# Performance work log

Measured on AMD Instinct MI355X. Metric: run time of the kernel, lower is better.

## Reference

```python
import jax, jax.numpy as jnp
import numpy as np

B, N, D, NFP, L = 4096, 64, 128, 2048, 3  # graphs, nodes/graph, emb_dim, vocab, layers


def setup_inputs() -> dict:
    key = jax.random.key(0)
    k0, k1, k2, k3, k4 = jax.random.split(key, 5)
    fps = jax.random.randint(k0, (B * N,), 0, NFP)            # node fingerprint ids, all graphs concatenated
    adj = jax.random.uniform(k1, (B, N, N), dtype=jnp.float32)  # per-graph adjacency blocks
    emb = jax.random.normal(k2, (NFP, D), dtype=jnp.float32) * 0.02
    W = jax.random.normal(k3, (L, D, D), dtype=jnp.float32) / np.sqrt(D).astype(np.float32)
    b = jax.random.normal(k4, (L, D), dtype=jnp.float32) * 0.01
    return {"fps": fps, "adj": adj, "emb": emb, "W": W, "b": b}


def reference(fps, adj, emb, W, b):
    # h = self.emb(fps): gather, then view as [B, N, D] so the block-diagonal
    # adjs.mm becomes an exact batched matmul over the true graph blocks.
    h = emb[fps].reshape(B, N, D)
    for l in range(L):
        # z = relu(W_l h + b_l); torch Linear is x @ W^T + b
        z = jax.nn.relu(jnp.einsum('bnd,kd->bnk', h, W[l]) + b[l])
        # h = z + adjs.mm(z), restricted to the diagonal blocks (same math)
        h = z + jnp.einsum('bmn,bnd->bmd', adj, z)
    # split by sz_list and sum each chunk -> per-graph sum pooling
    return h.sum(axis=1)  # [B, D]
```

## Files before the change

### kernel.cpp

```cpp
#include <hip/hip_runtime.h>

#define NGRAPH 4096
#define NNODE  64
#define NDIM   128
#define NLAYER 3
#define PH 136

typedef __attribute__((ext_vector_type(8))) short short8;
typedef __attribute__((ext_vector_type(4))) float f32x4;
typedef __bf16 bf16x2 __attribute__((ext_vector_type(2)));

union S8 { short8 s8; unsigned d[4]; };

static __device__ inline ushort f2bf(float f) {
  unsigned u = __float_as_uint(f);
  u += 0x7FFF + ((u >> 16) & 1);
  return (ushort)(u >> 16);
}

static __device__ inline unsigned pkbf(float x, float y) {
#if __has_builtin(__builtin_amdgcn_cvt_pk_bf16_f32)
  bf16x2 v = __builtin_amdgcn_cvt_pk_bf16_f32(x, y);
  return __builtin_bit_cast(unsigned, v);
#else
  return (unsigned)f2bf(x) | ((unsigned)f2bf(y) << 16);
#endif
}

__device__ __align__(16) ushort g_wbf[NLAYER * NDIM * NDIM];

__global__ __launch_bounds__(256) void convert_w(const float* __restrict__ W) {
  int i = blockIdx.x * 256 + threadIdx.x;
  g_wbf[i] = f2bf(W[i]);
}

__global__ __launch_bounds__(256, 4) void mpnn_mfma(
    const int* __restrict__ fps, const float* __restrict__ adj,
    const float* __restrict__ emb, const float* __restrict__ bias,
    float* __restrict__ out) {
  __shared__ __align__(16) ushort sh0[NNODE * PH];
  __shared__ __align__(16) ushort sh1[NNODE * PH];

  const int g    = blockIdx.x;
  const int t    = threadIdx.x;
  const int w    = t >> 6;
  const int lane = t & 63;
  const int r    = lane & 15;
  const int q    = lane >> 4;
  const int n0   = w << 5;

  const int addr0 = (r + 32 * (q & 1)) << 2;
  const int addr1 = addr0 + 64;
  const bool hiQ  = (q >= 2);

  const int* fg = fps + g * NNODE;
#pragma unroll
  for (int it = 0; it < 8; ++it) {
    int idx = it * 256 + t;
    int n = idx >> 5;
    int c = (idx & 31) << 2;
    float4 v = *(const float4*)(emb + fg[n] * NDIM + c);
    uint2 u = {pkbf(v.x, v.y), pkbf(v.z, v.w)};
    *(uint2*)(sh0 + n * PH + c) = u;
  }

  const float* adjg = adj + (size_t)g * NNODE * NNODE;
  short8 fadj[4][2];
#pragma unroll
  for (int nt = 0; nt < 4; ++nt) {
    int row = nt * 16 + r;
    const float* rp = adjg + row * NNODE;
#pragma unroll
    for (int kh = 0; kh < 2; ++kh) {
      int cb = kh * 32 + 8 * q;
      float4 v0 = *(const float4*)(rp + cb);
      float4 v1 = *(const float4*)(rp + cb + 4);
      float vv[8] = {v0.x, v0.y, v0.z, v0.w, v1.x, v1.y, v1.z, v1.w};
      if ((nt >> 1) == kh) {
#pragma unroll
        for (int j = 0; j < 8; ++j)
          if (row == cb + j) vv[j] += 1.0f;
      }
      S8 hi;
#pragma unroll
      for (int jp = 0; jp < 4; ++jp) hi.d[jp] = pkbf(vv[2 * jp], vv[2 * jp + 1]);
      fadj[nt][kh] = hi.s8;
    }
  }

  float bv[NLAYER][2];
#pragma unroll
  for (int l = 0; l < NLAYER; ++l)
#pragma unroll
    for (int nt = 0; nt < 2; ++nt) bv[l][nt] = bias[l * NDIM + n0 + nt * 16 + r];

  __syncthreads();

#pragma unroll 1
  for (int l = 0; l < NLAYER; ++l) {
    const ushort* shr = (l & 1) ? sh1 : sh0;
    ushort*       shw = (l & 1) ? sh0 : sh1;
    const ushort* Wl  = g_wbf + l * NDIM * NDIM;

    f32x4 acc[4][2];
#pragma unroll
    for (int nt = 0; nt < 2; ++nt) {
      float b = bv[l][nt];
#pragma unroll
      for (int mt = 0; mt < 4; ++mt) acc[mt][nt] = (f32x4){b, b, b, b};
    }
#pragma unroll
    for (int k0 = 0; k0 < NDIM; k0 += 32) {
      short8 bw0 = *(const short8*)(Wl + (n0 + r) * NDIM + k0 + 8 * q);
      short8 bw1 = *(const short8*)(Wl + (n0 + 16 + r) * NDIM + k0 + 8 * q);
#pragma unroll
      for (int mt = 0; mt < 4; ++mt) {
        short8 ah = *(const short8*)(shr + (mt * 16 + r) * PH + k0 + 8 * q);
        acc[mt][0] = __builtin_amdgcn_mfma_f32_16x16x32_bf16(ah, bw0, acc[mt][0], 0, 0, 0);
        acc[mt][1] = __builtin_amdgcn_mfma_f32_16x16x32_bf16(ah, bw1, acc[mt][1], 0, 0, 0);
      }
    }
    unsigned zc[4][2][2];
#pragma unroll
    for (int mt = 0; mt < 4; ++mt)
#pragma unroll
      for (int nt = 0; nt < 2; ++nt) {
        f32x4 a = acc[mt][nt];
        zc[mt][nt][0] = pkbf(fmaxf(a[0], 0.f), fmaxf(a[1], 0.f));
        zc[mt][nt][1] = pkbf(fmaxf(a[2], 0.f), fmaxf(a[3], 0.f));
      }

    f32x4 acc2[2][4];
#pragma unroll
    for (int mt = 0; mt < 2; ++mt)
#pragma unroll
      for (int nt = 0; nt < 4; ++nt) acc2[mt][nt] = (f32x4){0.f, 0.f, 0.f, 0.f};
#pragma unroll
    for (int kh = 0; kh < 2; ++kh) {
#pragma unroll
      for (int mt2 = 0; mt2 < 2; ++mt2) {
        S8 az;
#pragma unroll
        for (int p = 0; p < 4; ++p) {
          int comp = p & 1;
          int lo = __builtin_amdgcn_ds_bpermute((p < 2) ? addr0 : addr1,
                                                (int)zc[2 * kh][mt2][comp]);
          int hi = __builtin_amdgcn_ds_bpermute((p < 2) ? addr0 : addr1,
                                                (int)zc[2 * kh + 1][mt2][comp]);
          az.d[p] = (unsigned)(hiQ ? hi : lo);
        }
#pragma unroll
        for (int nt = 0; nt < 4; ++nt)
          acc2[mt2][nt] = __builtin_amdgcn_mfma_f32_16x16x32_bf16(az.s8, fadj[nt][kh], acc2[mt2][nt], 0, 0, 0);
      }
    }

    if (l < NLAYER - 1) {
#pragma unroll
      for (int mt2 = 0; mt2 < 2; ++mt2)
#pragma unroll
        for (int nt = 0; nt < 4; ++nt) {
          f32x4 a = acc2[mt2][nt];
          uint2 u = {pkbf(a[0], a[1]), pkbf(a[2], a[3])};
          *(uint2*)(shw + (nt * 16 + r) * PH + n0 + mt2 * 16 + 4 * q) = u;
        }
      __syncthreads();
    } else {
#pragma unroll
      for (int mt2 = 0; mt2 < 2; ++mt2) {
        f32x4 s;
#pragma unroll
        for (int i = 0; i < 4; ++i)
          s[i] = acc2[mt2][0][i] + acc2[mt2][1][i] + acc2[mt2][2][i] + acc2[mt2][3][i];
#pragma unroll
        for (int m = 1; m <= 8; m <<= 1) {
          s[0] += __shfl_xor(s[0], m);
          s[1] += __shfl_xor(s[1], m);
          s[2] += __shfl_xor(s[2], m);
          s[3] += __shfl_xor(s[3], m);
        }
        if (r == 0) {
          float4 o = {s[0], s[1], s[2], s[3]};
          *(float4*)(out + (size_t)g * NDIM + n0 + mt2 * 16 + 4 * q) = o;
        }
      }
    }
  }
}

extern "C" void kernel_launch(void* const* d_in, const int* in_sizes, int n_in,
                              void* d_out, int out_size, void* d_ws, size_t ws_size,
                              hipStream_t stream) {
  const int*   fps  = (const int*)d_in[0];
  const float* adj  = (const float*)d_in[1];
  const float* emb  = (const float*)d_in[2];
  const float* W    = (const float*)d_in[3];
  const float* bias = (const float*)d_in[4];
  float* out = (float*)d_out;

  hipLaunchKernelGGL(convert_w, dim3(192), dim3(256), 0, stream, W);
  hipLaunchKernelGGL(mpnn_mfma, dim3(NGRAPH), dim3(256), 0, stream,
                     fps, adj, emb, bias, out);
}
```

Before: 175.0 us.

## Use 8 waves per graph and stage adjacency in shared memory

```diff
diff --git a/kernel.cpp b/kernel.cpp
--- a/kernel.cpp
+++ b/kernel.cpp
@@ -5,6 +5,7 @@
 #define NDIM   128
 #define NLAYER 3
 #define PH 136
+#define PA 72
 
 typedef __attribute__((ext_vector_type(8))) short short8;
 typedef __attribute__((ext_vector_type(4))) float f32x4;
@@ -34,12 +35,13 @@
   g_wbf[i] = f2bf(W[i]);
 }
 
-__global__ __launch_bounds__(256, 4) void mpnn_mfma(
+__global__ __launch_bounds__(512, 6) void mpnn_mfma(
     const int* __restrict__ fps, const float* __restrict__ adj,
     const float* __restrict__ emb, const float* __restrict__ bias,
     float* __restrict__ out) {
   __shared__ __align__(16) ushort sh0[NNODE * PH];
   __shared__ __align__(16) ushort sh1[NNODE * PH];
+  __shared__ __align__(16) ushort sadj[NNODE * PA];
 
   const int g    = blockIdx.x;
   const int t    = threadIdx.x;
@@ -47,7 +49,7 @@
   const int lane = t & 63;
   const int r    = lane & 15;
   const int q    = lane >> 4;
-  const int n0   = w << 5;
+  const int n0   = w << 4;
 
   const int addr0 = (r + 32 * (q & 1)) << 2;
   const int addr1 = addr0 + 64;
@@ -55,8 +57,8 @@
 
   const int* fg = fps + g * NNODE;
 #pragma unroll
-  for (int it = 0; it < 8; ++it) {
-    int idx = it * 256 + t;
+  for (int it = 0; it < 4; ++it) {
+    int idx = it * 512 + t;
     int n = idx >> 5;
     int c = (idx & 31) << 2;
     float4 v = *(const float4*)(emb + fg[n] * NDIM + c);
@@ -65,34 +67,23 @@
   }
 
   const float* adjg = adj + (size_t)g * NNODE * NNODE;
-  short8 fadj[4][2];
 #pragma unroll
-  for (int nt = 0; nt < 4; ++nt) {
-    int row = nt * 16 + r;
-    const float* rp = adjg + row * NNODE;
-#pragma unroll
-    for (int kh = 0; kh < 2; ++kh) {
-      int cb = kh * 32 + 8 * q;
-      float4 v0 = *(const float4*)(rp + cb);
-      float4 v1 = *(const float4*)(rp + cb + 4);
-      float vv[8] = {v0.x, v0.y, v0.z, v0.w, v1.x, v1.y, v1.z, v1.w};
-      if ((nt >> 1) == kh) {
-#pragma unroll
-        for (int j = 0; j < 8; ++j)
-          if (row == cb + j) vv[j] += 1.0f;
-      }
-      S8 hi;
-#pragma unroll
-      for (int jp = 0; jp < 4; ++jp) hi.d[jp] = pkbf(vv[2 * jp], vv[2 * jp + 1]);
-      fadj[nt][kh] = hi.s8;
-    }
+  for (int it = 0; it < 2; ++it) {
+    int idx = it * 512 + t;
+    int n = idx >> 4;
+    int c = (idx & 15) << 2;
+    float4 v = *(const float4*)(adjg + n * NNODE + c);
+    v.x += (n == c + 0) ? 1.0f : 0.0f;
+    v.y += (n == c + 1) ? 1.0f : 0.0f;
+    v.z += (n == c + 2) ? 1.0f : 0.0f;
+    v.w += (n == c + 3) ? 1.0f : 0.0f;
+    uint2 u = {pkbf(v.x, v.y), pkbf(v.z, v.w)};
+    *(uint2*)(sadj + n * PA + c) = u;
   }
 
-  float bv[NLAYER][2];
+  float bv[NLAYER];
 #pragma unroll
-  for (int l = 0; l < NLAYER; ++l)
-#pragma unroll
-    for (int nt = 0; nt < 2; ++nt) bv[l][nt] = bias[l * NDIM + n0 + nt * 16 + r];
+  for (int l = 0; l < NLAYER; ++l) bv[l] = bias[l * NDIM + n0 + r];
 
   __syncthreads();
 
@@ -102,87 +93,71 @@
     ushort*       shw = (l & 1) ? sh0 : sh1;
     const ushort* Wl  = g_wbf + l * NDIM * NDIM;
 
-    f32x4 acc[4][2];
+    f32x4 acc[4];
 #pragma unroll
-    for (int nt = 0; nt < 2; ++nt) {
-      float b = bv[l][nt];
-#pragma unroll
-      for (int mt = 0; mt < 4; ++mt) acc[mt][nt] = (f32x4){b, b, b, b};
-    }
+    for (int mt = 0; mt < 4; ++mt) acc[mt] = (f32x4){bv[l], bv[l], bv[l], bv[l]};
 #pragma unroll
     for (int k0 = 0; k0 < NDIM; k0 += 32) {
-      short8 bw0 = *(const short8*)(Wl + (n0 + r) * NDIM + k0 + 8 * q);
-      short8 bw1 = *(const short8*)(Wl + (n0 + 16 + r) * NDIM + k0 + 8 * q);
+      short8 bw = *(const short8*)(Wl + (n0 + r) * NDIM + k0 + 8 * q);
 #pragma unroll
       for (int mt = 0; mt < 4; ++mt) {
         short8 ah = *(const short8*)(shr + (mt * 16 + r) * PH + k0 + 8 * q);
-        acc[mt][0] = __builtin_amdgcn_mfma_f32_16x16x32_bf16(ah, bw0, acc[mt][0], 0, 0, 0);
-        acc[mt][1] = __builtin_amdgcn_mfma_f32_16x16x32_bf16(ah, bw1, acc[mt][1], 0, 0, 0);
+        acc[mt] = __builtin_amdgcn_mfma_f32_16x16x32_bf16(ah, bw, acc[mt], 0, 0, 0);
       }
     }
-    unsigned zc[4][2][2];
+    unsigned zc[4][2];
 #pragma unroll
-    for (int mt = 0; mt < 4; ++mt)
+    for (int mt = 0; mt < 4; ++mt) {
+      f32x4 a = acc[mt];
+      zc[mt][0] = pkbf(fmaxf(a[0], 0.f), fmaxf(a[1], 0.f));
+      zc[mt][1] = pkbf(fmaxf(a[2], 0.f), fmaxf(a[3], 0.f));
+    }
+
+    f32x4 acc2[4];
 #pragma unroll
-      for (int nt = 0; nt < 2; ++nt) {
-        f32x4 a = acc[mt][nt];
-        zc[mt][nt][0] = pkbf(fmaxf(a[0], 0.f), fmaxf(a[1], 0.f));
-        zc[mt][nt][1] = pkbf(fmaxf(a[2], 0.f), fmaxf(a[3], 0.f));
-      }
-
-    f32x4 acc2[2][4];
-#pragma unroll
-    for (int mt = 0; mt < 2; ++mt)
-#pragma unroll
-      for (int nt = 0; nt < 4; ++nt) acc2[mt][nt] = (f32x4){0.f, 0.f, 0.f, 0.f};
+    for (int nt = 0; nt < 4; ++nt) acc2[nt] = (f32x4){0.f, 0.f, 0.f, 0.f};
 #pragma unroll
     for (int kh = 0; kh < 2; ++kh) {
+      S8 az;
 #pragma unroll
-      for (int mt2 = 0; mt2 < 2; ++mt2) {
-        S8 az;
+      for (int p = 0; p < 4; ++p) {
+        int comp = p & 1;
+        int lo = __builtin_amdgcn_ds_bpermute((p < 2) ? addr0 : addr1,
+                                              (int)zc[2 * kh][comp]);
+        int hi = __builtin_amdgcn_ds_bpermute((p < 2) ? addr0 : addr1,
+                                              (int)zc[2 * kh + 1][comp]);
+        az.d[p] = (unsigned)(hiQ ? hi : lo);
+      }
 #pragma unroll
-        for (int p = 0; p < 4; ++p) {
-          int comp = p & 1;
-          int lo = __builtin_amdgcn_ds_bpermute((p < 2) ? addr0 : addr1,
-                                                (int)zc[2 * kh][mt2][comp]);
-          int hi = __builtin_amdgcn_ds_bpermute((p < 2) ? addr0 : addr1,
-                                                (int)zc[2 * kh + 1][mt2][comp]);
-          az.d[p] = (unsigned)(hiQ ? hi : lo);
-        }
-#pragma unroll
-        for (int nt = 0; nt < 4; ++nt)
-          acc2[mt2][nt] = __builtin_amdgcn_mfma_f32_16x16x32_bf16(az.s8, fadj[nt][kh], acc2[mt2][nt], 0, 0, 0);
+      for (int nt = 0; nt < 4; ++nt) {
+        short8 fb = *(const short8*)(sadj + (nt * 16 + r) * PA + kh * 32 + 8 * q);
+        acc2[nt] = __builtin_amdgcn_mfma_f32_16x16x32_bf16(az.s8, fb, acc2[nt], 0, 0, 0);
       }
     }
 
     if (l < NLAYER - 1) {
 #pragma unroll
-      for (int mt2 = 0; mt2 < 2; ++mt2)
-#pragma unroll
-        for (int nt = 0; nt < 4; ++nt) {
-          f32x4 a = acc2[mt2][nt];
-          uint2 u = {pkbf(a[0], a[1]), pkbf(a[2], a[3])};
-          *(uint2*)(shw + (nt * 16 + r) * PH + n0 + mt2 * 16 + 4 * q) = u;
-        }
+      for (int nt = 0; nt < 4; ++nt) {
+        f32x4 a = acc2[nt];
+        uint2 u = {pkbf(a[0], a[1]), pkbf(a[2], a[3])};
+        *(uint2*)(shw + (nt * 16 + r) * PH + n0 + 4 * q) = u;
+      }
       __syncthreads();
     } else {
+      f32x4 s;
 #pragma unroll
-      for (int mt2 = 0; mt2 < 2; ++mt2) {
-        f32x4 s;
+      for (int i = 0; i < 4; ++i)
+        s[i] = acc2[0][i] + acc2[1][i] + acc2[2][i] + acc2[3][i];
 #pragma unroll
-        for (int i = 0; i < 4; ++i)
-          s[i] = acc2[mt2][0][i] + acc2[mt2][1][i] + acc2[mt2][2][i] + acc2[mt2][3][i];
-#pragma unroll
-        for (int m = 1; m <= 8; m <<= 1) {
-          s[0] += __shfl_xor(s[0], m);
-          s[1] += __shfl_xor(s[1], m);
-          s[2] += __shfl_xor(s[2], m);
-          s[3] += __shfl_xor(s[3], m);
-        }
-        if (r == 0) {
-          float4 o = {s[0], s[1], s[2], s[3]};
-          *(float4*)(out + (size_t)g * NDIM + n0 + mt2 * 16 + 4 * q) = o;
-        }
+      for (int m = 1; m <= 8; m <<= 1) {
+        s[0] += __shfl_xor(s[0], m);
+        s[1] += __shfl_xor(s[1], m);
+        s[2] += __shfl_xor(s[2], m);
+        s[3] += __shfl_xor(s[3], m);
+      }
+      if (r == 0) {
+        float4 o = {s[0], s[1], s[2], s[3]};
+        *(float4*)(out + (size_t)g * NDIM + n0 + 4 * q) = o;
       }
     }
   }
@@ -199,6 +174,6 @@
   float* out = (float*)d_out;
 
   hipLaunchKernelGGL(convert_w, dim3(192), dim3(256), 0, stream, W);
-  hipLaunchKernelGGL(mpnn_mfma, dim3(NGRAPH), dim3(256), 0, stream,
+  hipLaunchKernelGGL(mpnn_mfma, dim3(NGRAPH), dim3(512), 0, stream,
                      fps, adj, emb, bias, out);
 }
```

Result: faster. 163.2 us (-6.7%).
